# Optimization experiments

Hardware: AMD Instinct MI355X
Metric: run time of the kernel (lower is better)

## Reference

```python
import jax, jax.numpy as jnp
import numpy as np

def setup_inputs() -> dict:
    key = jax.random.key(0)
    k1, k2 = jax.random.split(key)
    B, T, J, d = 128, 2048, 128, 512
    U = jax.random.normal(k1, (B, J, d), dtype=jnp.float32)  # query encoding
    S = jax.random.normal(k2, (B, T, J), dtype=jnp.float32)  # similarity matrix
    return {"U": U, "S": S}

def reference(U, S):
    # a = softmax(S) over last (query) axis; out[b,t,:] = sum_j a[b,t,j] * U[b,j,:]
    # The original expand_dims/multiply/sum is algebraically a batched matmul.
    a = jax.nn.softmax(S, axis=-1)          # [B, T, J]
    return jnp.einsum('btj,bjd->btd', a, U)  # [B, T, d]
```

## Files before the change

### kernel.cpp

```cpp
#include <hip/hip_runtime.h>
#include <stdint.h>

typedef uint16_t u16;
typedef uint32_t u32;
typedef __attribute__((ext_vector_type(4))) int   int4v;
typedef __attribute__((ext_vector_type(4))) short short4v;
typedef __attribute__((ext_vector_type(8))) short short8;
typedef __attribute__((ext_vector_type(4))) float float4v;

__device__ __forceinline__ u16 f2bf(float f) {
  u32 x = __float_as_uint(f);
  x += 0x7fffu + ((x >> 16) & 1u);
  return (u16)(x >> 16);
}
__device__ __forceinline__ void llds16(const u16* g, u16* l) {
  __builtin_amdgcn_global_load_lds(
      (const __attribute__((address_space(1))) void*)g,
      (__attribute__((address_space(3))) void*)l, 16, 0, 0);
}

#define BB 128
#define TT 2048
#define JJ 128
#define DD 512

__global__ __launch_bounds__(256) void u_transpose(const float* __restrict__ U,
                                                   u16* __restrict__ Ut) {
  __shared__ u16 tile[128 * 72];
  const int t  = threadIdx.x;
  const int b  = blockIdx.x >> 3;
  const int d0 = (blockIdx.x & 7) << 6;
  const float* src = U + (size_t)b * (JJ * DD);
  u16* dst         = Ut + (size_t)b * (DD * JJ);
#pragma unroll
  for (int i = 0; i < 8; ++i) {
    int idx = i * 256 + t;
    int j = idx >> 4, c = idx & 15;
    float4v v = *(const float4v*)(src + (size_t)j * DD + d0 + c * 4);
    short4v p;
#pragma unroll
    for (int e = 0; e < 4; ++e) p[e] = (short)f2bf(v[e]);
    *(short4v*)(tile + j * 72 + c * 4) = p;
  }
  __syncthreads();
#pragma unroll
  for (int i = 0; i < 4; ++i) {
    int idx = i * 256 + t;
    int n = idx >> 4, cj = idx & 15;
    short8 vv;
#pragma unroll
    for (int k = 0; k < 8; ++k) vv[k] = (short)tile[(cj * 8 + k) * 72 + n];
    *(short8*)(dst + (size_t)(d0 + n) * JJ + cj * 8) = vv;
  }
}

__global__ __launch_bounds__(256, 2) void softmax_gemm(const float* __restrict__ S,
                                                       const u16* __restrict__ Ut,
                                                       float* __restrict__ O) {
  __shared__ __align__(16) u16 a_lds[128 * 128];
  __shared__ __align__(16) u16 b_lds[128 * 128];

  const int tid = threadIdx.x;
  const int bid = blockIdx.x;
  const int swz = (bid & 7) * 256 + (bid >> 3);
  const int b   = swz >> 4;
  const int tm  = swz & 15;
  const int wave = tid >> 6, lane = tid & 63;
  const int ml = lane & 15, quad = lane >> 4;
  const int wm = wave & 1, wn = wave >> 1;

  const u16* utb = Ut + (size_t)b * (DD * JJ);

#pragma unroll
  for (int i = 0; i < 8; ++i) {
    int ch = i * 256 + tid;
    int s = ch >> 9, n = (ch >> 2) & 127, qp = ch & 3;
    int c4 = qp ^ ((n >> 1) & 3);
    const u16* g = utb + n * JJ + s * 32 + c4 * 8;
    u16* l = b_lds + (size_t)(i * 256 + wave * 64) * 8;
    llds16(g, l);
  }

  int4v pf[8];
#pragma unroll
  for (int i = 0; i < 8; ++i) {
    int ch = i * 256 + tid;
    int s = ch >> 9, n = (ch >> 2) & 127, qp = ch & 3;
    int c4 = qp ^ ((n >> 1) & 3);
    pf[i] = *(const int4v*)(utb + (size_t)128 * JJ + n * JJ + s * 32 + c4 * 8);
  }

  const int m = tid >> 1, h = tid & 1;
  const float* srow = S + ((size_t)b * TT + tm * 128 + m) * JJ + h * 64;
  float x[64];
#pragma unroll
  for (int c = 0; c < 16; ++c) {
    float4v v = ((const float4v*)srow)[c];
#pragma unroll
    for (int e = 0; e < 4; ++e) x[c * 4 + e] = v[e];
  }
  float mx = -1e30f;
#pragma unroll
  for (int e = 0; e < 64; ++e) mx = fmaxf(mx, x[e]);
  mx = fmaxf(mx, __shfl_xor(mx, 1, 64));
  float sum = 0.f;
#pragma unroll
  for (int e = 0; e < 64; ++e) { x[e] = __expf(x[e] - mx); sum += x[e]; }
  sum += __shfl_xor(sum, 1, 64);
  const float rs = 1.0f / sum;
#pragma unroll
  for (int c = 0; c < 8; ++c) {
    short8 us;
#pragma unroll
    for (int e = 0; e < 8; ++e) us[e] = (short)f2bf(x[c * 8 + e] * rs);
    int s  = h * 2 + (c >> 2);
    int qp = (c & 3) ^ ((m >> 1) & 3);
    *(short8*)(a_lds + s * 4096 + m * 32 + qp * 8) = us;
  }

  __syncthreads();

  short8 av[4][4];
#pragma unroll
  for (int mi = 0; mi < 4; ++mi) {
    int mm = wm * 64 + mi * 16 + ml;
    int qp = quad ^ ((mm >> 1) & 3);
#pragma unroll
    for (int s = 0; s < 4; ++s)
      av[mi][s] = *(const short8*)(a_lds + s * 4096 + mm * 32 + qp * 8);
  }

  float* ob = O + ((size_t)b * TT + tm * 128) * DD;

#pragma unroll
  for (int tn = 0; tn < 4; ++tn) {
    float4v acc[4][4];
#pragma unroll
    for (int mi = 0; mi < 4; ++mi)
#pragma unroll
      for (int ni = 0; ni < 4; ++ni) {
        float4v z = {0.f, 0.f, 0.f, 0.f};
        acc[mi][ni] = z;
      }

#pragma unroll
    for (int s = 0; s < 4; ++s) {
      short8 bv[4];
#pragma unroll
      for (int ni = 0; ni < 4; ++ni) {
        int nn = wn * 64 + ni * 16 + ml;
        int qp = quad ^ ((nn >> 1) & 3);
        bv[ni] = *(const short8*)(b_lds + s * 4096 + nn * 32 + qp * 8);
      }
#pragma unroll
      for (int mi = 0; mi < 4; ++mi)
#pragma unroll
        for (int ni = 0; ni < 4; ++ni)
          acc[mi][ni] = __builtin_amdgcn_mfma_f32_16x16x32_bf16(
              bv[ni], av[mi][s], acc[mi][ni], 0, 0, 0);
    }

    if (tn < 3) {
      __syncthreads();
#pragma unroll
      for (int i = 0; i < 8; ++i) {
        int ch = i * 256 + tid;
        *(int4v*)(b_lds + (size_t)ch * 8) = pf[i];
      }
      __syncthreads();
      if (tn < 2) {
        const u16* utn = utb + (size_t)(tn + 2) * 128 * JJ;
#pragma unroll
        for (int i = 0; i < 8; ++i) {
          int ch = i * 256 + tid;
          int s = ch >> 9, n = (ch >> 2) & 127, qp = ch & 3;
          int c4 = qp ^ ((n >> 1) & 3);
          pf[i] = *(const int4v*)(utn + n * JJ + s * 32 + c4 * 8);
        }
      }
    }

#pragma unroll
    for (int mi = 0; mi < 4; ++mi) {
      const int t = wm * 64 + mi * 16 + ml;
#pragma unroll
      for (int ni = 0; ni < 4; ++ni) {
        const int d = tn * 128 + wn * 64 + ni * 16 + quad * 4;
        *(float4v*)(ob + (size_t)t * DD + d) = acc[mi][ni];
      }
    }
  }
}

extern "C" void kernel_launch(void* const* d_in, const int* in_sizes, int n_in,
                              void* d_out, int out_size, void* d_ws, size_t ws_size,
                              hipStream_t stream) {
  (void)in_sizes; (void)n_in; (void)out_size; (void)ws_size;
  const float* U = (const float*)d_in[0];
  const float* S = (const float*)d_in[1];
  float* out = (float*)d_out;
  u16* Ut    = (u16*)d_ws;

  u_transpose<<<BB * 8, 256, 0, stream>>>(U, Ut);
  softmax_gemm<<<BB * 16, 256, 0, stream>>>(S, Ut, out);
}
```

Measured before the change: 663.0 us.

## Load GEMM B operand directly from global memory instead of staging through LDS

Removes the LDS buffer for the transposed U tiles, along with its prefetch registers and the barriers around it. Each wave now reads its B fragments straight from global memory (expected to hit L2) inside the MFMA loop, and re-reads A fragments from LDS every k-step instead of holding them in registers. The aim is to cut LDS footprint and register pressure so three blocks fit per CU, raising occupancy. The cost is more global and LDS load traffic in the inner loop, with no software prefetch to hide its latency.

Result: slower. 695.9 us (+5.0%).

```diff
diff --git a/kernel.cpp b/kernel.cpp
--- a/kernel.cpp
+++ b/kernel.cpp
@@ -12,11 +12,6 @@
   u32 x = __float_as_uint(f);
   x += 0x7fffu + ((x >> 16) & 1u);
   return (u16)(x >> 16);
-}
-__device__ __forceinline__ void llds16(const u16* g, u16* l) {
-  __builtin_amdgcn_global_load_lds(
-      (const __attribute__((address_space(1))) void*)g,
-      (__attribute__((address_space(3))) void*)l, 16, 0, 0);
 }
 
 #define BB 128
@@ -54,11 +49,10 @@
   }
 }
 
-__global__ __launch_bounds__(256, 2) void softmax_gemm(const float* __restrict__ S,
+__global__ __launch_bounds__(256, 3) void softmax_gemm(const float* __restrict__ S,
                                                        const u16* __restrict__ Ut,
                                                        float* __restrict__ O) {
   __shared__ __align__(16) u16 a_lds[128 * 128];
-  __shared__ __align__(16) u16 b_lds[128 * 128];
 
   const int tid = threadIdx.x;
   const int bid = blockIdx.x;
@@ -70,25 +64,6 @@
   const int wm = wave & 1, wn = wave >> 1;
 
   const u16* utb = Ut + (size_t)b * (DD * JJ);
-
-#pragma unroll
-  for (int i = 0; i < 8; ++i) {
-    int ch = i * 256 + tid;
-    int s = ch >> 9, n = (ch >> 2) & 127, qp = ch & 3;
-    int c4 = qp ^ ((n >> 1) & 3);
-    const u16* g = utb + n * JJ + s * 32 + c4 * 8;
-    u16* l = b_lds + (size_t)(i * 256 + wave * 64) * 8;
-    llds16(g, l);
-  }
-
-  int4v pf[8];
-#pragma unroll
-  for (int i = 0; i < 8; ++i) {
-    int ch = i * 256 + tid;
-    int s = ch >> 9, n = (ch >> 2) & 127, qp = ch & 3;
-    int c4 = qp ^ ((n >> 1) & 3);
-    pf[i] = *(const int4v*)(utb + (size_t)128 * JJ + n * JJ + s * 32 + c4 * 8);
-  }
 
   const int m = tid >> 1, h = tid & 1;
   const float* srow = S + ((size_t)b * TT + tm * 128 + m) * JJ + h * 64;
@@ -120,19 +95,11 @@
 
   __syncthreads();
 
-  short8 av[4][4];
-#pragma unroll
-  for (int mi = 0; mi < 4; ++mi) {
-    int mm = wm * 64 + mi * 16 + ml;
-    int qp = quad ^ ((mm >> 1) & 3);
-#pragma unroll
-    for (int s = 0; s < 4; ++s)
-      av[mi][s] = *(const short8*)(a_lds + s * 4096 + mm * 32 + qp * 8);
-  }
-
   float* ob = O + ((size_t)b * TT + tm * 128) * DD;
 
-#pragma unroll
+  const u16* bv_base = utb + (size_t)(wn * 64 + ml) * JJ + quad * 8;
+
+#pragma unroll 1
   for (int tn = 0; tn < 4; ++tn) {
     float4v acc[4][4];
 #pragma unroll
@@ -143,41 +110,27 @@
         acc[mi][ni] = z;
       }
 
+    const u16* bv_tn = bv_base + (size_t)tn * 128 * JJ;
+
 #pragma unroll
     for (int s = 0; s < 4; ++s) {
       short8 bv[4];
 #pragma unroll
-      for (int ni = 0; ni < 4; ++ni) {
-        int nn = wn * 64 + ni * 16 + ml;
-        int qp = quad ^ ((nn >> 1) & 3);
-        bv[ni] = *(const short8*)(b_lds + s * 4096 + nn * 32 + qp * 8);
+      for (int ni = 0; ni < 4; ++ni)
+        bv[ni] = *(const short8*)(bv_tn + (size_t)ni * 16 * JJ + s * 32);
+      short8 av[4];
+#pragma unroll
+      for (int mi = 0; mi < 4; ++mi) {
+        int mm = wm * 64 + mi * 16 + ml;
+        int qp = quad ^ ((mm >> 1) & 3);
+        av[mi] = *(const short8*)(a_lds + s * 4096 + mm * 32 + qp * 8);
       }
 #pragma unroll
       for (int mi = 0; mi < 4; ++mi)
 #pragma unroll
         for (int ni = 0; ni < 4; ++ni)
           acc[mi][ni] = __builtin_amdgcn_mfma_f32_16x16x32_bf16(
-              bv[ni], av[mi][s], acc[mi][ni], 0, 0, 0);
-    }
-
-    if (tn < 3) {
-      __syncthreads();
-#pragma unroll
-      for (int i = 0; i < 8; ++i) {
-        int ch = i * 256 + tid;
-        *(int4v*)(b_lds + (size_t)ch * 8) = pf[i];
-      }
-      __syncthreads();
-      if (tn < 2) {
-        const u16* utn = utb + (size_t)(tn + 2) * 128 * JJ;
-#pragma unroll
-        for (int i = 0; i < 8; ++i) {
-          int ch = i * 256 + tid;
-          int s = ch >> 9, n = (ch >> 2) & 127, qp = ch & 3;
-          int c4 = qp ^ ((n >> 1) & 3);
-          pf[i] = *(const int4v*)(utn + n * JJ + s * 32 + c4 * 8);
-        }
-      }
+              bv[ni], av[mi], acc[mi][ni], 0, 0, 0);
     }
 
 #pragma unroll
```
